# Performance work log

Hardware: AMD Instinct MI355X
Metric: run time of the kernel (lower is better)

The kernel has to match this reference:

```python
import jax, jax.numpy as jnp
import numpy as np

DIM = 2048
H = 16       # num_heads
HKV = 4      # num_kv_heads
HD = DIM // H  # head_dim = 128
REP = H // HKV
ROPE_BASE = 10000.0
QK_GAIN_INIT = 1.0
B, T = 4, 2048


def rms_norm(x):
    # F.rms_norm with eps=None -> machine eps of dtype, no weight
    eps = jnp.finfo(x.dtype).eps
    return x * jax.lax.rsqrt(jnp.mean(x * x, axis=-1, keepdims=True) + eps)


def apply_rotary_emb(x, cos, sin):
    # x: [B, h, T, HD]; cos/sin: [T, HD//2]
    h = x.shape[-1] // 2
    x1, x2 = x[..., :h], x[..., h:]
    return jnp.concatenate((x1 * cos + x2 * sin, -x1 * sin + x2 * cos), axis=-1)


def setup_inputs() -> dict:
    key = jax.random.key(0)
    ks = jax.random.split(key, 6)
    kv_dim = HKV * HD
    x = jax.random.normal(ks[0], (B, T, DIM), dtype=jnp.float32)
    Wq = jax.random.normal(ks[1], (DIM, DIM), dtype=jnp.float32) * 0.02
    Wk = jax.random.normal(ks[2], (kv_dim, DIM), dtype=jnp.float32) * 0.02
    Wv = jax.random.normal(ks[3], (kv_dim, DIM), dtype=jnp.float32) * 0.02
    Wproj = jax.random.normal(ks[4], (DIM, DIM), dtype=jnp.float32) * 0.02
    q_gain = jnp.full((H,), QK_GAIN_INIT, dtype=jnp.float32)
    return {"x": x, "Wq": Wq, "Wk": Wk, "Wv": Wv, "Wproj": Wproj, "q_gain": q_gain}


def reference(x, Wq, Wk, Wv, Wproj, q_gain):
    Bs, Ts, D = x.shape
    # QKV projections (bias-free Linear: x @ W.T)
    q = (x @ Wq.T).reshape(Bs, Ts, H, HD).transpose(0, 2, 1, 3)      # [B,H,T,HD]
    k = (x @ Wk.T).reshape(Bs, Ts, HKV, HD).transpose(0, 2, 1, 3)    # [B,HKV,T,HD]
    v = (x @ Wv.T).reshape(Bs, Ts, HKV, HD).transpose(0, 2, 1, 3)
    # RMSNorm over head_dim
    q, k = rms_norm(q), rms_norm(k)
    # rotary
    inv_freq = 1.0 / (ROPE_BASE ** (jnp.arange(0, HD, 2, dtype=jnp.float32) / HD))
    t = jnp.arange(Ts, dtype=jnp.float32)
    freqs = jnp.outer(t, inv_freq)  # [T, HD//2]
    cos, sin = jnp.cos(freqs), jnp.sin(freqs)
    q = apply_rotary_emb(q, cos, sin)
    k = apply_rotary_emb(k, cos, sin)
    # per-head query gain
    q = q * q_gain[None, :, None, None]
    # GQA attention without materializing repeated K/V
    qg = q.reshape(Bs, HKV, REP, Ts, HD)
    scale = 1.0 / jnp.sqrt(jnp.asarray(HD, dtype=q.dtype))
    scores = jnp.einsum('bgrtd,bgsd->bgrts', qg, k) * scale  # [B,HKV,REP,T,T]
    causal = jnp.tril(jnp.ones((Ts, Ts), dtype=bool))
    scores = jnp.where(causal, scores, jnp.finfo(scores.dtype).min)
    attn = jax.nn.softmax(scores, axis=-1)
    y = jnp.einsum('bgrts,bgsd->bgrtd', attn, v)              # [B,HKV,REP,T,HD]
    y = y.reshape(Bs, H, Ts, HD).transpose(0, 2, 1, 3).reshape(Bs, Ts, D)
    return y @ Wproj.T
```

## Files before the change

kernel.cpp:

```cpp
#include <hip/hip_runtime.h>
#include <stdint.h>

typedef unsigned short u16;
typedef __attribute__((ext_vector_type(4))) float f32x4;
typedef __attribute__((ext_vector_type(8))) __bf16 bf16x8;
typedef __attribute__((ext_vector_type(4))) u16 u16x4;
typedef __attribute__((ext_vector_type(8))) u16 u16x8;

#define T_SEQ 2048
#define NB 4
#define NH 16
#define NKV 4
#define HDIM 128
#define PSTR 72

__device__ __forceinline__ u16 f2bf(float f) {
  __bf16 h = (__bf16)f;
  return __builtin_bit_cast(u16, h);
}
__device__ __forceinline__ float bf2f(u16 u) {
  union { uint32_t u; float f; } v; v.u = ((uint32_t)u) << 16;
  return v.f;
}
__device__ __forceinline__ void gload16(const void* g, void* l) {
  __builtin_amdgcn_global_load_lds((const __attribute__((address_space(1))) void*)g,
                                   (__attribute__((address_space(3))) void*)l, 16, 0, 0);
}
__device__ __forceinline__ f32x4 mfma16(bf16x8 a, bf16x8 b, f32x4 c) {
  return __builtin_amdgcn_mfma_f32_16x16x32_bf16(a, b, c, 0, 0, 0);
}

__global__ __launch_bounds__(256) void cvt_bf16(const float* __restrict__ in,
                                                u16* __restrict__ out, int n) {
  int idx = blockIdx.x * 256 + threadIdx.x;
  int stride = gridDim.x * 256;
  for (int i = idx * 4; i < n; i += stride * 4) {
    f32x4 v = *(const f32x4*)(in + i);
    u16x4 o;
    o[0] = f2bf(v[0]); o[1] = f2bf(v[1]); o[2] = f2bf(v[2]); o[3] = f2bf(v[3]);
    *(u16x4*)(out + i) = o;
  }
}

template <int MODE>
__global__ __launch_bounds__(256) void gemm128p3(const u16* __restrict__ A,
                                                 const u16* __restrict__ Bt,
                                                 u16* __restrict__ q_o, u16* __restrict__ k_o,
                                                 u16* __restrict__ v_o, float* __restrict__ f_o,
                                                 int K, int nx, int cpx) {
  __shared__ __align__(16) u16 As3[3 * 128 * 32];
  __shared__ __align__(16) u16 Bs3[3 * 128 * 32];
  const int tid = threadIdx.x;
  const int l = tid & 63, w = tid >> 6;
  const int l15 = l & 15, g16 = l >> 4;
  const int wr = w >> 1, wc = w & 1;

  const int oid = blockIdx.x + nx * blockIdx.y;
  const int wid = (oid & 7) * cpx + (oid >> 3);
  const int m0 = (wid / nx) * 128, n0 = (wid % nx) * 128;

  f32x4 acc[4][4] = {};

  const int row0 = tid >> 2, row1 = 64 + (tid >> 2), cc = tid & 3;
  const int sc0 = cc ^ ((row0 >> 1) & 3), sc1 = cc ^ ((row1 >> 1) & 3);
  const u16* pA0 = A + (size_t)(m0 + row0) * K + sc0 * 8;
  const u16* pA1 = A + (size_t)(m0 + row1) * K + sc1 * 8;
  const u16* pB0 = Bt + (size_t)(n0 + row0) * K + sc0 * 8;
  const u16* pB1 = Bt + (size_t)(n0 + row1) * K + sc1 * 8;

#define STAGE(buf)                                                   \
  {                                                                  \
    char* ab = (char*)As3 + (buf) * 8192 + w * 1024;                 \
    char* bb = (char*)Bs3 + (buf) * 8192 + w * 1024;                 \
    gload16(pA0, ab);                                                \
    gload16(pA1, ab + 4096);                                         \
    gload16(pB0, bb);                                                \
    gload16(pB1, bb + 4096);                                         \
    pA0 += 32; pA1 += 32; pB0 += 32; pB1 += 32;                      \
  }

#define COMPUTE(buf)                                                 \
  {                                                                  \
    const u16* AsB = As3 + (buf) * 4096;                             \
    const u16* BsB = Bs3 + (buf) * 4096;                             \
    bf16x8 af[4], bfr[4];                                            \
    _Pragma("unroll")                                                \
    for (int mt = 0; mt < 4; ++mt) {                                 \
      int arow = wr * 64 + mt * 16 + l15;                            \
      af[mt] = *(const bf16x8*)&AsB[arow * 32 +                      \
                                    ((g16 ^ ((arow >> 1) & 3)) * 8)];\
    }                                                                \
    _Pragma("unroll")                                                \
    for (int nt = 0; nt < 4; ++nt) {                                 \
      int brow = wc * 64 + nt * 16 + l15;                            \
      bfr[nt] = *(const bf16x8*)&BsB[brow * 32 +                     \
                                     ((g16 ^ ((brow >> 1) & 3)) * 8)];\
    }                                                                \
    __builtin_amdgcn_s_setprio(1);                                   \
    _Pragma("unroll")                                                \
    for (int mt = 0; mt < 4; ++mt)                                   \
      _Pragma("unroll")                                              \
      for (int nt = 0; nt < 4; ++nt)                                 \
        acc[mt][nt] = mfma16(af[mt], bfr[nt], acc[mt][nt]);          \
    __builtin_amdgcn_s_setprio(0);                                   \
  }

  const int ntiles = K >> 5;
  STAGE(0);
  STAGE(1);
  asm volatile("s_waitcnt vmcnt(4)" ::: "memory");
  __builtin_amdgcn_s_barrier();

  int cur = 0, nxt = 2;
  for (int t = 0; t < ntiles; ++t) {
    const bool more2 = (t + 2 < ntiles);
    if (more2) STAGE(nxt);
    COMPUTE(cur);
    if (t + 1 < ntiles) {
      if (more2) {
        asm volatile("s_waitcnt vmcnt(4)" ::: "memory");
      } else {
        asm volatile("s_waitcnt vmcnt(0)" ::: "memory");
      }
      __builtin_amdgcn_s_barrier();
    }
    cur = (cur == 2) ? 0 : cur + 1;
    nxt = (nxt == 2) ? 0 : nxt + 1;
  }
#undef STAGE
#undef COMPUTE

#pragma unroll
  for (int mt = 0; mt < 4; ++mt) {
#pragma unroll
    for (int r = 0; r < 4; ++r) {
      int row = m0 + wr * 64 + mt * 16 + g16 * 4 + r;
#pragma unroll
      for (int nt = 0; nt < 4; ++nt) {
        int n = n0 + wc * 64 + nt * 16 + l15;
        float val = acc[mt][nt][r];
        if (MODE == 1) {
          f_o[(size_t)row * 2048 + n] = val;
        } else {
          int b = row >> 11, t = row & (T_SEQ - 1);
          u16 bv = f2bf(val);
          if (n < 2048) {
            int h = n >> 7, d = n & 127;
            q_o[((size_t)(b * NH + h) * T_SEQ + t) * HDIM + d] = bv;
          } else if (n < 2560) {
            int n2 = n - 2048; int h = n2 >> 7, d = n2 & 127;
            k_o[((size_t)(b * NKV + h) * T_SEQ + t) * HDIM + d] = bv;
          } else {
            int n2 = n - 2560; int h = n2 >> 7, d = n2 & 127;
            v_o[((size_t)(b * NKV + h) * T_SEQ + t) * HDIM + d] = bv;
          }
        }
      }
    }
  }
}

__global__ __launch_bounds__(256) void rmsrope(u16* __restrict__ buf,
                                               const float* __restrict__ gains,
                                               int nheads, float fold, int useGain) {
  const int w = threadIdx.x >> 6, l = threadIdx.x & 63;
  const int rid = blockIdx.x * 4 + w;
  const int t = rid & (T_SEQ - 1);
  const int h = (rid >> 11) % nheads;
  u16* p = buf + (size_t)rid * HDIM;
  float x1 = bf2f(p[l]), x2 = bf2f(p[l + 64]);
  float ss = x1 * x1 + x2 * x2;
#pragma unroll
  for (int m = 32; m; m >>= 1) ss += __shfl_xor(ss, m, 64);
  float rn = rsqrtf(ss * (1.0f / 128.0f) + 1.1920928955078125e-7f);
  float g = useGain ? gains[h] * fold : fold;
  float sc = rn * g;
  float inv = exp2f(-(float)l * (13.287712379549449f / 64.0f));
  float ang = (float)t * inv;
  float s, c;
  __sincosf(ang, &s, &c);
  float o1 = (x1 * c + x2 * s) * sc;
  float o2 = (x2 * c - x1 * s) * sc;
  p[l] = f2bf(o1);
  p[l + 64] = f2bf(o2);
}

__global__ __launch_bounds__(256) void vtrans(const u16* __restrict__ in,
                                              u16* __restrict__ out) {
  __shared__ u16 tileT[64][PSTR];
  const int tid = threadIdx.x;
  const int t0 = blockIdx.x * 64, d0 = blockIdx.y * 64, bg = blockIdx.z;
  const int row = tid >> 2, c0 = (tid & 3) * 16;
  const u16* src = in + ((size_t)bg * T_SEQ + t0 + row) * HDIM + d0 + c0;
  u16x8 a = *(const u16x8*)src;
  u16x8 bb = *(const u16x8*)(src + 8);
#pragma unroll
  for (int j = 0; j < 8; ++j) {
    tileT[c0 + j][row] = a[j];
    tileT[c0 + 8 + j][row] = bb[j];
  }
  __syncthreads();
  u16* dst = out + ((size_t)bg * HDIM + d0 + row) * T_SEQ + t0 + c0;
  *(u16x8*)dst = *(const u16x8*)&tileT[row][c0];
  *(u16x8*)(dst + 8) = *(const u16x8*)&tileT[row][c0 + 8];
}

__global__ __launch_bounds__(256) void attn_fwd3(const u16* __restrict__ qb,
                                                 const u16* __restrict__ kb,
                                                 const u16* __restrict__ vtb,
                                                 u16* __restrict__ yb,
                                                 const float* __restrict__ gains) {
  __shared__ __align__(16) u16 Ks[64 * 128];
  __shared__ __align__(16) u16 Vs[128 * 64];
  __shared__ __align__(16) u16 Ps[4][32 * PSTR];

  const int tid = threadIdx.x, l = tid & 63, w = tid >> 6;
  const int l16 = l & 15, g16 = l >> 4;

  const int oid = blockIdx.x + 8 * blockIdx.y;
  const int wid = (oid & 7) * 64 + (oid >> 3);
  const int pair = wid & 7, bh = wid >> 3;
  const int b = bh >> 4, h = bh & 15, gr = h >> 2;

  const float Mh = 16.33f * fabsf(gains[h]) + 0.5f;
  const u16* kbase = kb + (size_t)(b * NKV + gr) * T_SEQ * HDIM;
  const u16* vtbase = vtb + (size_t)(b * NKV + gr) * HDIM * T_SEQ;

  for (int phase = 0; phase < 2; ++phase) {
    const int qt = phase ? (15 - pair) : pair;
    const int q0 = qt * 128 + w * 32;
    const int qhi = q0 + 31;

    bf16x8 qf[2][4];
    const u16* qbase = qb + ((size_t)bh * T_SEQ + q0) * HDIM;
#pragma unroll
    for (int nf = 0; nf < 2; ++nf)
#pragma unroll
      for (int s = 0; s < 4; ++s)
        qf[nf][s] = *(const bf16x8*)(qbase + (size_t)(nf * 16 + l16) * HDIM + s * 32 + g16 * 8);

    f32x4 oacc[2][8] = {};
    float den[2] = {0.f, 0.f};
    const int ntile = 2 * qt + 2;

    for (int kt = 0; kt < ntile; ++kt) {
#pragma unroll
      for (int r = 0; r < 4; ++r) {
        int c = r * 256 + tid;
        int row = c >> 4, c16 = c & 15;
        int sc = c16 ^ (row & 7);
        gload16(kbase + ((size_t)(kt * 64 + row)) * HDIM + sc * 8,
                (char*)Ks + (r * 256 + w * 64) * 16);
      }
#pragma unroll
      for (int r = 0; r < 4; ++r) {
        int c = r * 256 + tid;
        int row = c >> 3, c8 = c & 7;
        int sc = c8 ^ (row & 7);
        gload16(vtbase + (size_t)row * T_SEQ + kt * 64 + sc * 8,
                (char*)Vs + (r * 256 + w * 64) * 16);
      }
      __syncthreads();

      if (kt * 64 <= qhi) {
        f32x4 sacc[4][2] = {};
        __builtin_amdgcn_s_setprio(1);
#pragma unroll
        for (int mt = 0; mt < 4; ++mt) {
          int key = mt * 16 + l16;
#pragma unroll
          for (int s = 0; s < 4; ++s) {
            bf16x8 kf = *(const bf16x8*)&Ks[key * 128 + ((s * 4 + g16) ^ (key & 7)) * 8];
#pragma unroll
            for (int nf = 0; nf < 2; ++nf)
              sacc[mt][nf] = mfma16(kf, qf[nf][s], sacc[mt][nf]);
          }
        }
        __builtin_amdgcn_s_setprio(0);

        const bool diagcross = (kt * 64 + 63 > q0);
#pragma unroll
        for (int mt = 0; mt < 4; ++mt) {
          int keyb = kt * 64 + mt * 16 + g16 * 4;
#pragma unroll
          for (int nf = 0; nf < 2; ++nf) {
            u16x4 p4;
#pragma unroll
            for (int r = 0; r < 4; ++r) {
              float pv = exp2f(sacc[mt][nf][r] - Mh);
              if (diagcross && (keyb + r > q0 + nf * 16 + l16)) pv = 0.f;
              den[nf] += pv;
              p4[r] = f2bf(pv);
            }
            *(u16x4*)&Ps[w][(nf * 16 + l16) * PSTR + mt * 16 + g16 * 4] = p4;
          }
        }

        __builtin_amdgcn_s_setprio(1);
#pragma unroll
        for (int ks = 0; ks < 2; ++ks) {
          bf16x8 pa[2];
#pragma unroll
          for (int mq = 0; mq < 2; ++mq)
            pa[mq] = *(const bf16x8*)&Ps[w][(mq * 16 + l16) * PSTR + ks * 32 + g16 * 8];
#pragma unroll
          for (int dt = 0; dt < 8; ++dt) {
            int d = dt * 16 + l16;
            bf16x8 vv = *(const bf16x8*)&Vs[d * 64 + (((ks * 4 + g16) ^ (d & 7)) * 8)];
#pragma unroll
            for (int mq = 0; mq < 2; ++mq)
              oacc[mq][dt] = mfma16(pa[mq], vv, oacc[mq][dt]);
          }
        }
        __builtin_amdgcn_s_setprio(0);
      }
      __syncthreads();
    }

#pragma unroll
    for (int nf = 0; nf < 2; ++nf) {
      den[nf] += __shfl_xor(den[nf], 16, 64);
      den[nf] += __shfl_xor(den[nf], 32, 64);
    }
    float rden[2][4];
#pragma unroll
    for (int mq = 0; mq < 2; ++mq)
#pragma unroll
      for (int r = 0; r < 4; ++r)
        rden[mq][r] = 1.f / __shfl(den[mq], g16 * 4 + r, 64);

#pragma unroll
    for (int mq = 0; mq < 2; ++mq)
#pragma unroll
      for (int dt = 0; dt < 8; ++dt)
#pragma unroll
        for (int r = 0; r < 4; ++r) {
          int t = q0 + mq * 16 + g16 * 4 + r;
          int d = dt * 16 + l16;
          yb[(((size_t)b * T_SEQ + t) * NH + h) * HDIM + d] = f2bf(oacc[mq][dt][r] * rden[mq][r]);
        }
    __syncthreads();
  }
}

extern "C" void kernel_launch(void* const* d_in, const int* in_sizes, int n_in,
                              void* d_out, int out_size, void* d_ws, size_t ws_size,
                              hipStream_t stream) {
  const float* x = (const float*)d_in[0];
  const float* Wq = (const float*)d_in[1];
  const float* Wk = (const float*)d_in[2];
  const float* Wv = (const float*)d_in[3];
  const float* Wproj = (const float*)d_in[4];
  const float* qg = (const float*)d_in[5];
  float* out = (float*)d_out;

  u16* xbf = (u16*)d_ws;
  u16* Wqkv = xbf + (size_t)8192 * 2048;
  u16* Wpj = Wqkv + (size_t)3072 * 2048;
  u16* qbuf = Wpj + (size_t)2048 * 2048;
  u16* kbuf = qbuf + (size_t)8192 * 2048;
  u16* vbuf = kbuf + (size_t)2048 * 2048;
  u16* ybuf = xbf;
  u16* vtbuf = Wqkv;

  cvt_bf16<<<8192, 256, 0, stream>>>(x, xbf, 8192 * 2048);
  cvt_bf16<<<4096, 256, 0, stream>>>(Wq, Wqkv, 2048 * 2048);
  cvt_bf16<<<1024, 256, 0, stream>>>(Wk, Wqkv + (size_t)2048 * 2048, 512 * 2048);
  cvt_bf16<<<1024, 256, 0, stream>>>(Wv, Wqkv + (size_t)2560 * 2048, 512 * 2048);
  cvt_bf16<<<4096, 256, 0, stream>>>(Wproj, Wpj, 2048 * 2048);

  gemm128p3<0><<<dim3(24, 64), 256, 0, stream>>>(xbf, Wqkv, qbuf, kbuf, vbuf, nullptr,
                                                 2048, 24, 192);

  rmsrope<<<32768, 256, 0, stream>>>(qbuf, qg, NH,
                                     1.4426950408889634f / 11.313708498984761f, 1);
  rmsrope<<<8192, 256, 0, stream>>>(kbuf, nullptr, NKV, 1.0f, 0);
  vtrans<<<dim3(32, 2, 16), 256, 0, stream>>>(vbuf, vtbuf);

  attn_fwd3<<<dim3(8, 64), 256, 0, stream>>>(qbuf, kbuf, vtbuf, ybuf, qg);

  gemm128p3<1><<<dim3(16, 64), 256, 0, stream>>>(ybuf, Wpj, nullptr, nullptr, nullptr, out,
                                                 2048, 16, 128);
}
```

Before: 387.4 us.

## Add 256x256-tile GEMM kernel for output projection and shrink convert grids

Adds a new 512-thread GEMM kernel with 256x256 output tiles. It double-buffers 64-wide K slices in LDS with an XOR swizzle and raises wave priority around the MFMA block. The output projection now uses this kernel, 256 blocks in a single wave over the CUs, in place of the 128-tile kernel. The larger tile is meant to cut global reloads of A and B per output element. The trade-offs are 128KB of LDS per block, so only one block fits per CU, and heavier register pressure. The bf16 conversion launches for x, Wq and Wproj also use fewer blocks.

```diff
diff --git a/kernel.cpp b/kernel.cpp
--- a/kernel.cpp
+++ b/kernel.cpp
@@ -160,6 +160,120 @@
   }
 }
 
+template <int MODE>
+__global__ __launch_bounds__(512, 2) void gemm256(const u16* __restrict__ A,
+                                                  const u16* __restrict__ Bt,
+                                                  u16* __restrict__ q_o, u16* __restrict__ k_o,
+                                                  u16* __restrict__ v_o, float* __restrict__ f_o,
+                                                  int K, int ntn, int cpx) {
+  __shared__ __align__(16) u16 As[2][256 * 64];
+  __shared__ __align__(16) u16 Bs[2][256 * 64];
+  const int tid = threadIdx.x;
+  const int l = tid & 63, w = tid >> 6;
+  const int l16 = l & 15, g16 = l >> 4;
+  const int wr = w >> 2, wc = w & 3;
+
+  const int oid = blockIdx.x;
+  const int wid = (oid & 7) * cpx + (oid >> 3);
+  const int m0 = (wid / ntn) * 256, n0 = (wid % ntn) * 256;
+
+  f32x4 acc[8][4] = {};
+
+  const int srow = tid >> 3, scc = tid & 7;
+  const u16* pA[4];
+  const u16* pB[4];
+#pragma unroll
+  for (int j = 0; j < 4; ++j) {
+    int row = j * 64 + srow;
+    int cc = scc ^ (row & 7);
+    pA[j] = A + (size_t)(m0 + row) * K + cc * 8;
+    pB[j] = Bt + (size_t)(n0 + row) * K + cc * 8;
+  }
+
+#define STAGE(buf)                                              \
+  {                                                             \
+    char* ab = (char*)As[buf] + w * 1024;                       \
+    char* bb = (char*)Bs[buf] + w * 1024;                       \
+    _Pragma("unroll")                                           \
+    for (int j = 0; j < 4; ++j) {                               \
+      gload16(pA[j], ab + j * 8192);                            \
+      pA[j] += 64;                                              \
+    }                                                           \
+    _Pragma("unroll")                                           \
+    for (int j = 0; j < 4; ++j) {                               \
+      gload16(pB[j], bb + j * 8192);                            \
+      pB[j] += 64;                                              \
+    }                                                           \
+  }
+
+  const int ntk = K >> 6;
+  STAGE(0);
+  __syncthreads();
+
+  for (int t = 0; t < ntk; ++t) {
+    const int buf = t & 1;
+    if (t + 1 < ntk) STAGE(buf ^ 1);
+#pragma unroll
+    for (int ks = 0; ks < 2; ++ks) {
+      bf16x8 bfr[4];
+#pragma unroll
+      for (int nf = 0; nf < 4; ++nf) {
+        int brow = wc * 64 + nf * 16 + l16;
+        int slot = (ks * 4 + g16) ^ (brow & 7);
+        bfr[nf] = *(const bf16x8*)&Bs[buf][brow * 64 + slot * 8];
+      }
+#pragma unroll
+      for (int rh = 0; rh < 2; ++rh) {
+        bf16x8 af[4];
+#pragma unroll
+        for (int f = 0; f < 4; ++f) {
+          int arow = wr * 128 + rh * 64 + f * 16 + l16;
+          int slot = (ks * 4 + g16) ^ (arow & 7);
+          af[f] = *(const bf16x8*)&As[buf][arow * 64 + slot * 8];
+        }
+        __builtin_amdgcn_s_setprio(1);
+#pragma unroll
+        for (int f = 0; f < 4; ++f)
+#pragma unroll
+          for (int nf = 0; nf < 4; ++nf)
+            acc[rh * 4 + f][nf] = mfma16(af[f], bfr[nf], acc[rh * 4 + f][nf]);
+        __builtin_amdgcn_s_setprio(0);
+      }
+    }
+    __syncthreads();
+  }
+#undef STAGE
+
+#pragma unroll
+  for (int rf = 0; rf < 8; ++rf) {
+#pragma unroll
+    for (int rr = 0; rr < 4; ++rr) {
+      int row = m0 + wr * 128 + rf * 16 + g16 * 4 + rr;
+#pragma unroll
+      for (int nf = 0; nf < 4; ++nf) {
+        int n = n0 + wc * 64 + nf * 16 + l16;
+        float val = acc[rf][nf][rr];
+        if (MODE == 1) {
+          f_o[(size_t)row * 2048 + n] = val;
+        } else {
+          int b = row >> 11, t = row & (T_SEQ - 1);
+          u16 bv = f2bf(val);
+          if (n < 2048) {
+            int h = n >> 7, d = n & 127;
+            q_o[((size_t)(b * NH + h) * T_SEQ + t) * HDIM + d] = bv;
+          } else if (n < 2560) {
+            int n2 = n - 2048; int h = n2 >> 7, d = n2 & 127;
+            k_o[((size_t)(b * NKV + h) * T_SEQ + t) * HDIM + d] = bv;
+          } else {
+            int n2 = n - 2560; int h = n2 >> 7, d = n2 & 127;
+            v_o[((size_t)(b * NKV + h) * T_SEQ + t) * HDIM + d] = bv;
+          }
+        }
+      }
+    }
+  }
+}
+
 __global__ __launch_bounds__(256) void rmsrope(u16* __restrict__ buf,
                                                const float* __restrict__ gains,
                                                int nheads, float fold, int useGain) {
@@ -363,11 +477,11 @@
   u16* ybuf = xbf;
   u16* vtbuf = Wqkv;
 
-  cvt_bf16<<<8192, 256, 0, stream>>>(x, xbf, 8192 * 2048);
-  cvt_bf16<<<4096, 256, 0, stream>>>(Wq, Wqkv, 2048 * 2048);
+  cvt_bf16<<<2048, 256, 0, stream>>>(x, xbf, 8192 * 2048);
+  cvt_bf16<<<2048, 256, 0, stream>>>(Wq, Wqkv, 2048 * 2048);
   cvt_bf16<<<1024, 256, 0, stream>>>(Wk, Wqkv + (size_t)2048 * 2048, 512 * 2048);
   cvt_bf16<<<1024, 256, 0, stream>>>(Wv, Wqkv + (size_t)2560 * 2048, 512 * 2048);
-  cvt_bf16<<<4096, 256, 0, stream>>>(Wproj, Wpj, 2048 * 2048);
+  cvt_bf16<<<2048, 256, 0, stream>>>(Wproj, Wpj, 2048 * 2048);
 
   gemm128p3<0><<<dim3(24, 64), 256, 0, stream>>>(xbf, Wqkv, qbuf, kbuf, vbuf, nullptr,
                                                  2048, 24, 192);
@@ -379,6 +493,5 @@
 
   attn_fwd3<<<dim3(8, 64), 256, 0, stream>>>(qbuf, kbuf, vtbuf, ybuf, qg);
 
-  gemm128p3<1><<<dim3(16, 64), 256, 0, stream>>>(ybuf, Wpj, nullptr, nullptr, nullptr, out,
-                                                 2048, 16, 128);
-}
+  gemm256<1><<<256, 512, 0, stream>>>(ybuf, Wpj, nullptr, nullptr, nullptr, out, 2048, 8, 32);
+}
```

Result: faster. 361.6 us (-6.7%).
